# Kernel tuning notes

Measured on AMD Instinct MI355X. Metric: run time of the kernel, lower is better.

The kernel has to match this reference:

```python
import jax, jax.numpy as jnp
import numpy as np

D_MODEL = 1024
N_HEADS = 16
D_K = D_MODEL // N_HEADS


def setup_inputs() -> dict:
    key = jax.random.key(0)
    ks = jax.random.split(key, 9)
    B, S = 2, 2048
    scale = 1.0 / np.sqrt(D_MODEL)
    inp = {
        "X": jax.random.normal(ks[0], (B, S, D_MODEL), dtype=jnp.float32),
        "Wq": jax.random.normal(ks[1], (D_MODEL, D_MODEL), dtype=jnp.float32) * scale,
        "bq": jnp.zeros((D_MODEL,), dtype=jnp.float32),
        "Wk": jax.random.normal(ks[2], (D_MODEL, D_MODEL), dtype=jnp.float32) * scale,
        "bk": jnp.zeros((D_MODEL,), dtype=jnp.float32),
        "Wv": jax.random.normal(ks[3], (D_MODEL, D_MODEL), dtype=jnp.float32) * scale,
        "bv": jnp.zeros((D_MODEL,), dtype=jnp.float32),
        "Wo": jax.random.normal(ks[4], (D_MODEL, D_MODEL), dtype=jnp.float32) * scale,
        "bo": jnp.zeros((D_MODEL,), dtype=jnp.float32),
    }
    return inp


def reference(X, Wq, bq, Wk, bk, Wv, bv, Wo, bo):
    B, S, _ = X.shape
    # QKV projections (torch Linear: x @ W.T + b; here W stored as [in, out])
    Q = X @ Wq + bq
    K = X @ Wk + bk
    V = X @ Wv + bv
    # [B, S, H, Dk] -> [B, H, S, Dk]
    def split_heads(t):
        return t.reshape(B, S, N_HEADS, D_K).transpose(0, 2, 1, 3)
    Q, K, V = split_heads(Q), split_heads(K), split_heads(V)
    scores = jnp.einsum('bhqd,bhkd->bhqk', Q, K) / jnp.sqrt(jnp.float32(D_K))
    attn = jax.nn.softmax(scores, axis=-1)
    out = jnp.einsum('bhqk,bhkd->bhqd', attn, V)  # [B, H, S, Dk]
    out = out.transpose(0, 2, 1, 3).reshape(B, S, D_MODEL)
    return out @ Wo + bo
```

## Files before the change

### kernel.cpp

```cpp
#include <hip/hip_runtime.h>
#include <hip/hip_bf16.h>


typedef __attribute__((ext_vector_type(8))) short short8;
typedef __attribute__((ext_vector_type(4))) float f32x4;
typedef __attribute__((ext_vector_type(2))) float f32x2;
typedef unsigned short u16;
typedef unsigned int u32;

static __device__ __forceinline__ u16 f2bf(float f) {
    union { float f; u32 u; } c; c.f = f;
    u32 u = c.u;
    u32 r = u + 0x7fffu + ((u >> 16) & 1u);
    return (u16)(r >> 16);
}
static __device__ __forceinline__ float bf2f(u16 x) {
    union { u32 u; float f; } c; c.u = ((u32)x) << 16;
    return c.f;
}

#define GL1(p) ((const __attribute__((address_space(1))) void*)(p))
#define LD3(p) ((__attribute__((address_space(3))) void*)(p))
static __device__ __forceinline__ void gld16(const void* g, void* l) {
    __builtin_amdgcn_global_load_lds(GL1(g), LD3(l), 16, 0, 0);
}

#define Q_PRESCALE 0.18033688011112042f

__global__ __launch_bounds__(256) void prep(
    const float* __restrict__ X, u16* __restrict__ Xb,
    const float* __restrict__ Wq, const float* __restrict__ Wk,
    const float* __restrict__ Wv, const float* __restrict__ Wo,
    const float* __restrict__ bq, const float* __restrict__ bk,
    const float* __restrict__ bv,
    u16* __restrict__ Wqkv, u16* __restrict__ Wto, float* __restrict__ Bp)
{
    int id = blockIdx.x;
    int t = threadIdx.x;
    if (id == 5120) {
        for (int i = t; i < 3072; i += 256) {
            int wsel = i >> 10, c = i & 1023;
            float v = (wsel == 0) ? bq[c] * Q_PRESCALE : (wsel == 1 ? bk[c] : bv[c]);
            Bp[i] = v;
        }
        return;
    }
    if (id >= 1024) {
        int i = (id - 1024) * 1024 + t * 4;
        float4 v = *reinterpret_cast<const float4*>(X + i);
        ushort4 o;
        o.x = f2bf(v.x); o.y = f2bf(v.y); o.z = f2bf(v.z); o.w = f2bf(v.w);
        *reinterpret_cast<ushort4*>(Xb + i) = o;
        return;
    }
    int which = id >> 8;
    const float* W; u16* T; float sc;
    switch (which) {
        case 0: W = Wq; T = Wqkv;                sc = Q_PRESCALE; break;
        case 1: W = Wk; T = Wqkv + 1024 * 1024;  sc = 1.0f; break;
        case 2: W = Wv; T = Wqkv + 2048 * 1024;  sc = 1.0f; break;
        default: W = Wo; T = Wto;                sc = 1.0f; break;
    }
    int rem = id & 255;
    int n0 = (rem & 15) * 64, k0 = (rem >> 4) * 64;
    __shared__ float tile[64][65];
    int r = t / 16, c4 = (t % 16) * 4;
    #pragma unroll
    for (int p = 0; p < 4; p++) {
        int row = p * 16 + r;
        float4 v = *reinterpret_cast<const float4*>(W + (k0 + row) * 1024 + n0 + c4);
        tile[row][c4 + 0] = v.x * sc; tile[row][c4 + 1] = v.y * sc;
        tile[row][c4 + 2] = v.z * sc; tile[row][c4 + 3] = v.w * sc;
    }
    __syncthreads();
    #pragma unroll
    for (int p = 0; p < 4; p++) {
        int nrow = p * 16 + r;
        ushort4 o;
        o.x = f2bf(tile[c4 + 0][nrow]); o.y = f2bf(tile[c4 + 1][nrow]);
        o.z = f2bf(tile[c4 + 2][nrow]); o.w = f2bf(tile[c4 + 3][nrow]);
        *reinterpret_cast<ushort4*>(T + (n0 + nrow) * 1024 + k0 + c4) = o;
    }
}

__global__ __launch_bounds__(256, 3) void gemm_qkv(
    const u16* __restrict__ Xb, const u16* __restrict__ Wqkv,
    const float* __restrict__ Bp,
    u16* __restrict__ Qb, u16* __restrict__ Kb, u16* __restrict__ Vtg)
{
    __shared__ __align__(16) u16 As[2][128 * 32];
    __shared__ __align__(16) u16 Bs[2][128 * 32];
    int t = threadIdx.x;
    int w = t >> 6, lane = t & 63, l15 = lane & 15, quad = lane >> 4;
    int wm = (w >> 1) * 64, wn = (w & 1) * 64;
    int bid = blockIdx.x;
    int row0 = (bid & 31) * 128, col0 = (bid >> 5) * 128;

    int drow = lane >> 2;
    int gc8 = ((lane & 3) ^ (drow & 3) ^ ((drow >> 2) & 3)) * 8;
    int asw = ((quad ^ (l15 & 3) ^ ((l15 >> 2) & 3)) & 3) * 8;

    const u16* Ag = Xb + (row0 + drow) * 1024 + gc8;
    const u16* Bg = Wqkv + (col0 + drow) * 1024 + gc8;

    f32x4 acc[4][4];
    #pragma unroll
    for (int i = 0; i < 4; i++)
        #pragma unroll
        for (int j = 0; j < 4; j++)
            acc[i][j] = (f32x4){0.f, 0.f, 0.f, 0.f};

    #pragma unroll
    for (int q = 0; q < 2; q++) {
        int rr = w * 32 + q * 16;
        gld16(Ag + rr * 1024, &As[0][rr * 32]);
        gld16(Bg + rr * 1024, &Bs[0][rr * 32]);
    }
    for (int kt = 0; kt < 32; kt++) {
        __syncthreads();
        int cur = kt & 1;
        if (kt < 31) {
            int k0 = (kt + 1) * 32;
            #pragma unroll
            for (int q = 0; q < 2; q++) {
                int rr = w * 32 + q * 16;
                gld16(Ag + rr * 1024 + k0, &As[cur ^ 1][rr * 32]);
                gld16(Bg + rr * 1024 + k0, &Bs[cur ^ 1][rr * 32]);
            }
        }
        short8 a[4], b[4];
        #pragma unroll
        for (int i = 0; i < 4; i++)
            a[i] = *reinterpret_cast<const short8*>(&As[cur][(wm + i * 16 + l15) * 32 + asw]);
        #pragma unroll
        for (int j = 0; j < 4; j++)
            b[j] = *reinterpret_cast<const short8*>(&Bs[cur][(wn + j * 16 + l15) * 32 + asw]);
        #pragma unroll
        for (int i = 0; i < 4; i++)
            #pragma unroll
            for (int j = 0; j < 4; j++)
                acc[i][j] = __builtin_amdgcn_mfma_f32_16x16x32_bf16(a[i], b[j], acc[i][j], 0, 0, 0);
    }

    int osel = col0 >> 10;
    if (osel == 2) {
        #pragma unroll
        for (int i = 0; i < 4; i++) {
            int gr = row0 + wm + i * 16 + quad * 4;
            int b_ = gr >> 11, s = gr & 2047;
            #pragma unroll
            for (int j = 0; j < 4; j++) {
                int col = col0 + wn + j * 16 + l15;
                int c = col & 1023, h = c >> 6, d = c & 63;
                float bb = Bp[col];
                ushort4 pk;
                pk.x = f2bf(acc[i][j][0] + bb);
                pk.y = f2bf(acc[i][j][1] + bb);
                pk.z = f2bf(acc[i][j][2] + bb);
                pk.w = f2bf(acc[i][j][3] + bb);
                *reinterpret_cast<ushort4*>(&Vtg[((b_ * 16 + h) * 64 + d) * 2048 + s]) = pk;
            }
        }
    } else {
        u16* dst = osel ? Kb : Qb;
        #pragma unroll
        for (int i = 0; i < 4; i++) {
            int rowb = row0 + wm + i * 16 + quad * 4;
            #pragma unroll
            for (int j = 0; j < 4; j++) {
                int col = col0 + wn + j * 16 + l15;
                int c = col & 1023, h = c >> 6, d = c & 63;
                float bb = Bp[col];
                #pragma unroll
                for (int r = 0; r < 4; r++) {
                    int gr = rowb + r;
                    int b_ = gr >> 11, s = gr & 2047;
                    dst[(((b_ << 4) + h) * 2048 + s) * 64 + d] = f2bf(acc[i][j][r] + bb);
                }
            }
        }
    }
}

__global__ __launch_bounds__(256) void attn(
    const u16* __restrict__ Qb, const u16* __restrict__ Kb,
    const u16* __restrict__ Vtg, u16* __restrict__ Opart, float* __restrict__ Lsum)
{
    int bid = blockIdx.x;
    int bh = bid & 31, sp = (bid >> 5) & 3, qt = bid >> 7;
    int b_ = bh >> 4, h = bh & 15;
    const u16* Qp = Qb + bh * (2048 * 64);
    const u16* Kp = Kb + bh * (2048 * 64);
    const u16* Vp = Vtg + bh * (64 * 2048);
    u16* Op = Opart + sp * (4096 * 1024);
    float* Lp = Lsum + sp * (32 * 2048) + bh * 2048;

    __shared__ __align__(16) u16 Ks[64 * 64];
    __shared__ __align__(16) u16 Vt[64 * 64];
    __shared__ __align__(16) u16 Ps[128 * 64];

    int t = threadIdx.x, w = t >> 6, lane = t & 63, l15 = lane & 15, quad = lane >> 4;

    short8 qf[2][2];
    #pragma unroll
    for (int f = 0; f < 2; f++)
        #pragma unroll
        for (int ds = 0; ds < 2; ds++)
            qf[f][ds] = *reinterpret_cast<const short8*>(
                &Qp[(qt * 128 + w * 32 + f * 16 + l15) * 64 + ds * 32 + quad * 8]);

    int di = lane >> 3;
    int dc8 = ((lane & 7) ^ di) * 8;

    int rl = l15 & 7, rh = l15 >> 3;
    int koff[4][2];
    #pragma unroll
    for (int j = 0; j < 4; j++)
        #pragma unroll
        for (int ds = 0; ds < 2; ds++)
            koff[j][ds] = (j * 2 + rh) * 512 + rl * 64 + (((ds * 4 + quad) ^ rl) & 7) * 8;

    int pwt[2][4];
    #pragma unroll
    for (int f = 0; f < 2; f++)
        #pragma unroll
        for (int j = 0; j < 4; j++)
            pwt[f][j] = (w * 32 + f * 16 + l15) * 64 +
                        (((2 * j + (quad >> 1)) ^ rl) * 8) + (quad & 1) * 4;
    int prt[2][2];
    #pragma unroll
    for (int f = 0; f < 2; f++)
        #pragma unroll
        for (int ks = 0; ks < 2; ks++)
            prt[f][ks] = (w * 32 + f * 16 + l15) * 64 + (((4 * ks + quad) ^ rl) * 8);

    f32x4 acc[2][4];
    f32x2 lsum2[2] = {(f32x2){0.f, 0.f}, (f32x2){0.f, 0.f}};
    #pragma unroll
    for (int f = 0; f < 2; f++)
        #pragma unroll
        for (int j = 0; j < 4; j++) acc[f][j] = (f32x4){0.f, 0.f, 0.f, 0.f};

    int kb0 = sp * 512;
    for (int kt = 0; kt < 8; kt++) {
        int kbase = kb0 + kt * 64;
        __syncthreads();
        #pragma unroll
        for (int sg = 0; sg < 2; sg++) {
            int seg = w * 2 + sg;
            gld16(&Kp[(kbase + seg * 8 + di) * 64 + dc8], &Ks[seg * 512]);
            gld16(&Vp[(seg * 8 + di) * 2048 + kbase + dc8], &Vt[seg * 512]);
        }
        __syncthreads();

        f32x4 sc[2][4];
        #pragma unroll
        for (int j = 0; j < 4; j++) {
            f32x4 s0 = (f32x4){0.f, 0.f, 0.f, 0.f};
            f32x4 s1 = (f32x4){0.f, 0.f, 0.f, 0.f};
            #pragma unroll
            for (int ds = 0; ds < 2; ds++) {
                short8 kf = *reinterpret_cast<const short8*>(&Ks[koff[j][ds]]);
                s0 = __builtin_amdgcn_mfma_f32_16x16x32_bf16(kf, qf[0][ds], s0, 0, 0, 0);
                s1 = __builtin_amdgcn_mfma_f32_16x16x32_bf16(kf, qf[1][ds], s1, 0, 0, 0);
            }
            sc[0][j] = s0; sc[1][j] = s1;
        }

        #pragma unroll
        for (int f = 0; f < 2; f++)
            #pragma unroll
            for (int j = 0; j < 4; j++) {
                float p0 = __builtin_amdgcn_exp2f(sc[f][j][0]);
                float p1 = __builtin_amdgcn_exp2f(sc[f][j][1]);
                float p2 = __builtin_amdgcn_exp2f(sc[f][j][2]);
                float p3 = __builtin_amdgcn_exp2f(sc[f][j][3]);
                lsum2[f] += (f32x2){p0, p1};
                lsum2[f] += (f32x2){p2, p3};
                union { float fv; u32 uv; } c0, c1, c2, c3;
                c0.fv = p0; c1.fv = p1; c2.fv = p2; c3.fv = p3;
                uint2 pk;
                pk.x = (c0.uv >> 16) | (c1.uv & 0xffff0000u);
                pk.y = (c2.uv >> 16) | (c3.uv & 0xffff0000u);
                *reinterpret_cast<uint2*>(&Ps[pwt[f][j]]) = pk;
            }

        #pragma unroll
        for (int ks = 0; ks < 2; ks++) {
            short8 pf0 = *reinterpret_cast<const short8*>(&Ps[prt[0][ks]]);
            short8 pf1 = *reinterpret_cast<const short8*>(&Ps[prt[1][ks]]);
            #pragma unroll
            for (int j = 0; j < 4; j++) {
                short8 vf = *reinterpret_cast<const short8*>(&Vt[koff[j][ks]]);
                acc[0][j] = __builtin_amdgcn_mfma_f32_16x16x32_bf16(pf0, vf, acc[0][j], 0, 0, 0);
                acc[1][j] = __builtin_amdgcn_mfma_f32_16x16x32_bf16(pf1, vf, acc[1][j], 0, 0, 0);
            }
        }
    }

    #pragma unroll
    for (int f = 0; f < 2; f++) {
        float s = lsum2[f].x + lsum2[f].y;
        s += __shfl_xor(s, 16);
        s += __shfl_xor(s, 32);
        if (quad == 0)
            Lp[qt * 128 + w * 32 + f * 16 + l15] = s;
    }

    #pragma unroll
    for (int f = 0; f < 2; f++)
        #pragma unroll
        for (int j = 0; j < 4; j++)
            #pragma unroll
            for (int r = 0; r < 4; r++) {
                int srow = qt * 128 + w * 32 + f * 16 + quad * 4 + r;
                Op[(b_ * 2048 + srow) * 1024 + h * 64 + j * 16 + l15] = f2bf(acc[f][j][r]);
            }
}

__global__ __launch_bounds__(256) void combine(
    const u16* __restrict__ Op, const float* __restrict__ Ls,
    u16* __restrict__ Ob)
{
    int idx8 = (blockIdx.x * 256 + threadIdx.x) * 8;
    int row = idx8 >> 10, col = idx8 & 1023;
    int b_ = row >> 11, s = row & 2047, h = col >> 6;
    int li = (b_ * 16 + h) * 2048 + s;
    float l = Ls[li] + Ls[li + 65536] + Ls[li + 131072] + Ls[li + 196608];
    float inv = 1.0f / l;
    float accv[8];
    #pragma unroll
    for (int i = 0; i < 8; i++) accv[i] = 0.f;
    #pragma unroll
    for (int p = 0; p < 4; p++) {
        union { uint4 v; u16 s[8]; } ua;
        ua.v = *reinterpret_cast<const uint4*>(&Op[p * 4194304 + idx8]);
        #pragma unroll
        for (int i = 0; i < 8; i++) accv[i] += bf2f(ua.s[i]);
    }
    union { uint4 v; u16 s[8]; } uo;
    #pragma unroll
    for (int i = 0; i < 8; i++) uo.s[i] = f2bf(accv[i] * inv);
    *reinterpret_cast<uint4*>(&Ob[idx8]) = uo.v;
}

__global__ __launch_bounds__(256, 3) void gemm_out(
    const u16* __restrict__ Ob, const u16* __restrict__ Wto,
    const float* __restrict__ bo, float* __restrict__ out)
{
    __shared__ __align__(16) u16 As[2][128 * 32];
    __shared__ __align__(16) u16 Bs[2][128 * 32];
    int t = threadIdx.x;
    int w = t >> 6, lane = t & 63, l15 = lane & 15, quad = lane >> 4;
    int wm = (w >> 1) * 64, wn = (w & 1) * 64;
    int bid = blockIdx.x;
    int row0 = (bid & 31) * 128, col0 = (bid >> 5) * 128;

    int drow = lane >> 2;
    int gc8 = ((lane & 3) ^ (drow & 3) ^ ((drow >> 2) & 3)) * 8;
    int asw = ((quad ^ (l15 & 3) ^ ((l15 >> 2) & 3)) & 3) * 8;

    const u16* Ag = Ob + (row0 + drow) * 1024 + gc8;
    const u16* Bg = Wto + (col0 + drow) * 1024 + gc8;

    f32x4 acc[4][4];
    #pragma unroll
    for (int i = 0; i < 4; i++)
        #pragma unroll
        for (int j = 0; j < 4; j++)
            acc[i][j] = (f32x4){0.f, 0.f, 0.f, 0.f};

    #pragma unroll
    for (int q = 0; q < 2; q++) {
        int rr = w * 32 + q * 16;
        gld16(Ag + rr * 1024, &As[0][rr * 32]);
        gld16(Bg + rr * 1024, &Bs[0][rr * 32]);
    }
    for (int kt = 0; kt < 32; kt++) {
        __syncthreads();
        int cur = kt & 1;
        if (kt < 31) {
            int k0 = (kt + 1) * 32;
            #pragma unroll
            for (int q = 0; q < 2; q++) {
                int rr = w * 32 + q * 16;
                gld16(Ag + rr * 1024 + k0, &As[cur ^ 1][rr * 32]);
                gld16(Bg + rr * 1024 + k0, &Bs[cur ^ 1][rr * 32]);
            }
        }
        short8 a[4], b[4];
        #pragma unroll
        for (int i = 0; i < 4; i++)
            a[i] = *reinterpret_cast<const short8*>(&As[cur][(wm + i * 16 + l15) * 32 + asw]);
        #pragma unroll
        for (int j = 0; j < 4; j++)
            b[j] = *reinterpret_cast<const short8*>(&Bs[cur][(wn + j * 16 + l15) * 32 + asw]);
        #pragma unroll
        for (int i = 0; i < 4; i++)
            #pragma unroll
            for (int j = 0; j < 4; j++)
                acc[i][j] = __builtin_amdgcn_mfma_f32_16x16x32_bf16(a[i], b[j], acc[i][j], 0, 0, 0);
    }
    #pragma unroll
    for (int i = 0; i < 4; i++) {
        int rowb = row0 + wm + i * 16 + quad * 4;
        #pragma unroll
        for (int j = 0; j < 4; j++) {
            int col = col0 + wn + j * 16 + l15;
            float bb = bo[col];
            #pragma unroll
            for (int r = 0; r < 4; r++)
                out[(rowb + r) * 1024 + col] = acc[i][j][r] + bb;
        }
    }
}

extern "C" void kernel_launch(void* const* d_in, const int* in_sizes, int n_in,
                              void* d_out, int out_size, void* d_ws, size_t ws_size,
                              hipStream_t stream) {
    const float* X  = (const float*)d_in[0];
    const float* Wq = (const float*)d_in[1];
    const float* bq = (const float*)d_in[2];
    const float* Wk = (const float*)d_in[3];
    const float* bk = (const float*)d_in[4];
    const float* Wv = (const float*)d_in[5];
    const float* bv = (const float*)d_in[6];
    const float* Wo = (const float*)d_in[7];
    const float* bo = (const float*)d_in[8];
    float* out = (float*)d_out;

    char* ws = (char*)d_ws;
    u16* Xb    = (u16*)(ws);
    u16* Ob    = (u16*)(ws);
    u16* Wqkv  = (u16*)(ws + (8u  << 20));
    u16* Wto   = (u16*)(ws + (14u << 20));
    float* Bp  = (float*)(ws + (16u << 20));
    u16* Qb    = (u16*)(ws + (17u << 20));
    u16* Kb    = (u16*)(ws + (25u << 20));
    u16* Vtg   = (u16*)(ws + (33u << 20));
    u16* Op    = (u16*)(ws + (41u << 20));
    float* Ls  = (float*)(ws + (73u << 20));

    prep     <<<5121, 256, 0, stream>>>(X, Xb, Wq, Wk, Wv, Wo, bq, bk, bv, Wqkv, Wto, Bp);
    gemm_qkv <<<768, 256, 0, stream>>>(Xb, Wqkv, Bp, Qb, Kb, Vtg);
    attn     <<<2048, 256, 0, stream>>>(Qb, Kb, Vtg, Op, Ls);
    combine  <<<2048, 256, 0, stream>>>(Op, Ls, Ob);
    gemm_out <<<256, 256, 0, stream>>>(Ob, Wto, bo, out);
}
```

Baseline: 202.1 us.

## Double-buffer K/V tiles in attention loop and raise MFMA wave priority

The attention kernel now keeps two LDS buffers for the K and V tiles. It issues the async global-to-LDS loads for the next key tile before computing on the current one, so a loop iteration needs one barrier instead of two. It also wraps the MFMA sections in s_setprio to favour matrix work when waves are interleaved. The cost is doubled K/V LDS use, which may lower occupancy. The loop runs only eight iterations per block, so there is little room to hide latency.

```diff
diff --git a/kernel.cpp b/kernel.cpp
--- a/kernel.cpp
+++ b/kernel.cpp
@@ -195,8 +195,8 @@
     u16* Op = Opart + sp * (4096 * 1024);
     float* Lp = Lsum + sp * (32 * 2048) + bh * 2048;
 
-    __shared__ __align__(16) u16 Ks[64 * 64];
-    __shared__ __align__(16) u16 Vt[64 * 64];
+    __shared__ __align__(16) u16 Ks[2][64 * 64];
+    __shared__ __align__(16) u16 Vt[2][64 * 64];
     __shared__ __align__(16) u16 Ps[128 * 64];
 
     int t = threadIdx.x, w = t >> 6, lane = t & 63, l15 = lane & 15, quad = lane >> 4;
@@ -242,30 +242,40 @@
         for (int j = 0; j < 4; j++) acc[f][j] = (f32x4){0.f, 0.f, 0.f, 0.f};
 
     int kb0 = sp * 512;
+
+#define ISSUE_KV(KB, PB)                                                    \
+    {                                                                       \
+        _Pragma("unroll")                                                   \
+        for (int sg = 0; sg < 2; sg++) {                                    \
+            int seg = w * 2 + sg;                                           \
+            gld16(&Kp[((KB) + seg * 8 + di) * 64 + dc8], &Ks[PB][seg * 512]); \
+            gld16(&Vp[(seg * 8 + di) * 2048 + (KB) + dc8], &Vt[PB][seg * 512]); \
+        }                                                                   \
+    }
+
+    ISSUE_KV(kb0, 0);
+    __syncthreads();
+
     for (int kt = 0; kt < 8; kt++) {
-        int kbase = kb0 + kt * 64;
-        __syncthreads();
-        #pragma unroll
-        for (int sg = 0; sg < 2; sg++) {
-            int seg = w * 2 + sg;
-            gld16(&Kp[(kbase + seg * 8 + di) * 64 + dc8], &Ks[seg * 512]);
-            gld16(&Vp[(seg * 8 + di) * 2048 + kbase + dc8], &Vt[seg * 512]);
-        }
-        __syncthreads();
+        int cur = kt & 1;
+        if (kt < 7)
+            ISSUE_KV(kb0 + (kt + 1) * 64, cur ^ 1);
 
         f32x4 sc[2][4];
+        __builtin_amdgcn_s_setprio(1);
         #pragma unroll
         for (int j = 0; j < 4; j++) {
             f32x4 s0 = (f32x4){0.f, 0.f, 0.f, 0.f};
             f32x4 s1 = (f32x4){0.f, 0.f, 0.f, 0.f};
             #pragma unroll
             for (int ds = 0; ds < 2; ds++) {
-                short8 kf = *reinterpret_cast<const short8*>(&Ks[koff[j][ds]]);
+                short8 kf = *reinterpret_cast<const short8*>(&Ks[cur][koff[j][ds]]);
                 s0 = __builtin_amdgcn_mfma_f32_16x16x32_bf16(kf, qf[0][ds], s0, 0, 0, 0);
                 s1 = __builtin_amdgcn_mfma_f32_16x16x32_bf16(kf, qf[1][ds], s1, 0, 0, 0);
             }
             sc[0][j] = s0; sc[1][j] = s1;
         }
+        __builtin_amdgcn_s_setprio(0);
 
         #pragma unroll
         for (int f = 0; f < 2; f++)
@@ -285,18 +295,23 @@
                 *reinterpret_cast<uint2*>(&Ps[pwt[f][j]]) = pk;
             }
 
+        __builtin_amdgcn_s_setprio(1);
         #pragma unroll
         for (int ks = 0; ks < 2; ks++) {
             short8 pf0 = *reinterpret_cast<const short8*>(&Ps[prt[0][ks]]);
             short8 pf1 = *reinterpret_cast<const short8*>(&Ps[prt[1][ks]]);
             #pragma unroll
             for (int j = 0; j < 4; j++) {
-                short8 vf = *reinterpret_cast<const short8*>(&Vt[koff[j][ks]]);
+                short8 vf = *reinterpret_cast<const short8*>(&Vt[cur][koff[j][ks]]);
                 acc[0][j] = __builtin_amdgcn_mfma_f32_16x16x32_bf16(pf0, vf, acc[0][j], 0, 0, 0);
                 acc[1][j] = __builtin_amdgcn_mfma_f32_16x16x32_bf16(pf1, vf, acc[1][j], 0, 0, 0);
             }
         }
-    }
+        __builtin_amdgcn_s_setprio(0);
+
+        __syncthreads();
+    }
+#undef ISSUE_KV
 
     #pragma unroll
     for (int f = 0; f < 2; f++) {
```

Result: slower. 211.5 us (+4.7%).

## Prefetch next K/V tiles during softmax and PV phases, add MFMA priority

Applied to the files above, without the earlier changes.

The attention inner loop no longer loads K and V at the top of each iteration behind a pair of barriers. The next K tile is now issued right after the QK^T MFMAs finish reading Ks, and the next V tile right after the PV MFMAs finish reading Vt. This lets the global-to-LDS loads overlap the exp/pack and PV compute. s_setprio raises wave priority around the MFMA blocks. Nothing waits on the async loads explicitly, so correctness relies on the barrier at the start of each phase covering them.

```diff
diff --git a/kernel.cpp b/kernel.cpp
--- a/kernel.cpp
+++ b/kernel.cpp
@@ -242,18 +242,31 @@
         for (int j = 0; j < 4; j++) acc[f][j] = (f32x4){0.f, 0.f, 0.f, 0.f};
 
     int kb0 = sp * 512;
+
+#define ISSUE_K(KB)                                                          \
+    {                                                                        \
+        _Pragma("unroll")                                                    \
+        for (int sg = 0; sg < 2; sg++) {                                     \
+            int seg = w * 2 + sg;                                            \
+            gld16(&Kp[((KB) + seg * 8 + di) * 64 + dc8], &Ks[seg * 512]);    \
+        }                                                                    \
+    }
+#define ISSUE_V(KB)                                                          \
+    {                                                                        \
+        _Pragma("unroll")                                                    \
+        for (int sg = 0; sg < 2; sg++) {                                     \
+            int seg = w * 2 + sg;                                            \
+            gld16(&Vp[(seg * 8 + di) * 2048 + (KB) + dc8], &Vt[seg * 512]);  \
+        }                                                                    \
+    }
+
+    ISSUE_K(kb0);
+    ISSUE_V(kb0);
+    __syncthreads();
+
     for (int kt = 0; kt < 8; kt++) {
-        int kbase = kb0 + kt * 64;
-        __syncthreads();
-        #pragma unroll
-        for (int sg = 0; sg < 2; sg++) {
-            int seg = w * 2 + sg;
-            gld16(&Kp[(kbase + seg * 8 + di) * 64 + dc8], &Ks[seg * 512]);
-            gld16(&Vp[(seg * 8 + di) * 2048 + kbase + dc8], &Vt[seg * 512]);
-        }
-        __syncthreads();
-
         f32x4 sc[2][4];
+        __builtin_amdgcn_s_setprio(1);
         #pragma unroll
         for (int j = 0; j < 4; j++) {
             f32x4 s0 = (f32x4){0.f, 0.f, 0.f, 0.f};
@@ -266,6 +279,11 @@
             }
             sc[0][j] = s0; sc[1][j] = s1;
         }
+        __builtin_amdgcn_s_setprio(0);
+
+        __syncthreads();
+        if (kt < 7)
+            ISSUE_K(kb0 + (kt + 1) * 64);
 
         #pragma unroll
         for (int f = 0; f < 2; f++)
@@ -285,6 +303,7 @@
                 *reinterpret_cast<uint2*>(&Ps[pwt[f][j]]) = pk;
             }
 
+        __builtin_amdgcn_s_setprio(1);
         #pragma unroll
         for (int ks = 0; ks < 2; ks++) {
             short8 pf0 = *reinterpret_cast<const short8*>(&Ps[prt[0][ks]]);
@@ -296,7 +315,14 @@
                 acc[1][j] = __builtin_amdgcn_mfma_f32_16x16x32_bf16(pf1, vf, acc[1][j], 0, 0, 0);
             }
         }
-    }
+        __builtin_amdgcn_s_setprio(0);
+
+        __syncthreads();
+        if (kt < 7)
+            ISSUE_V(kb0 + (kt + 1) * 64);
+    }
+#undef ISSUE_K
+#undef ISSUE_V
 
     #pragma unroll
     for (int f = 0; f < 2; f++) {
```

After: 202.3 us. About the same (+0.1%).
